# Performance work log

Measured on AMD Instinct MI355X. Metric: run time of the kernel, lower is better.

The kernel has to match this reference:

```python
import jax, jax.numpy as jnp
import numpy as np

B, C, W, H = 2, 64, 96, 96


def _conv1x1(Wm, b, x):
    # 1x1 conv == per-pixel channel mixing: (O,C) x (B,C,W,H) -> (B,O,W,H)
    return jnp.einsum('oc,bchw->bohw', Wm, x) + b[None, :, None, None]


def setup_inputs() -> dict:
    key = jax.random.key(0)
    ks = jax.random.split(key, 12)
    s = 1.0 / np.sqrt(C)
    inp = {
        'x': jax.random.normal(ks[0], (B, C, W, H), jnp.float32),
        'y': jax.random.normal(ks[1], (B, C, W, H), jnp.float32),
        'Wq': jax.random.normal(ks[2], (C, C), jnp.float32) * s,
        'bq': jax.random.normal(ks[3], (C,), jnp.float32) * 0.01,
        'Wk': jax.random.normal(ks[4], (C, C), jnp.float32) * s,
        'bk': jax.random.normal(ks[5], (C,), jnp.float32) * 0.01,
        'Wvx': jax.random.normal(ks[6], (C, C), jnp.float32) * s,
        'bvx': jax.random.normal(ks[7], (C,), jnp.float32) * 0.01,
        'Wvy': jax.random.normal(ks[8], (C, C), jnp.float32) * s,
        'bvy': jax.random.normal(ks[9], (C,), jnp.float32) * 0.01,
        'gamma': jax.random.normal(ks[10], (1,), jnp.float32) * 0.1,
        'beta': jax.random.normal(ks[11], (1,), jnp.float32) * 0.1,
    }
    return inp


def reference(x, y, Wq, bq, Wk, bk, Wvx, bvx, Wvy, bvy, gamma, beta):
    b, c, w, h = x.shape
    n = w * h
    # Q from y, K from x (cross-query structure of the original module)
    q = _conv1x1(Wq, bq, y).reshape(b, c, n)          # (B,C,N)
    k = _conv1x1(Wk, bk, x).reshape(b, c, n)          # (B,C,N)
    energy = jnp.einsum('bcm,bcn->bmn', q, k)         # (B,N,N), query rows m
    attention = jax.nn.softmax(energy, axis=-1)       # softmax over keys n
    vx = _conv1x1(Wvx, bvx, x).reshape(b, c, n)       # (B,C,N)
    vy = _conv1x1(Wvy, bvy, y).reshape(b, c, n)
    # torch: bmm(value, attention^T) -> out[:, :, m] = sum_n value[:, :, n] * att[m, n]
    out_x = jnp.einsum('bcn,bmn->bcm', vx, attention).reshape(b, c, w, h)
    out_y = jnp.einsum('bcn,bmn->bcm', vy, attention).reshape(b, c, w, h)
    x_att = gamma[0] * out_x
    y_att = beta[0] * out_y
    return (x_att, y_att)
```

## Files before the change

### kernel.cpp

```cpp
#include <hip/hip_runtime.h>
#include <cstdint>
#include <cstddef>

#define BN 2
#define CC 64
#define NN 9216
#define KT 64
#define L2E 1.44269504088896340736f
#define M0L2 63.478581798f

typedef __attribute__((ext_vector_type(8))) _Float16 half8;
typedef __attribute__((ext_vector_type(2))) __fp16 fp16x2;
typedef __attribute__((ext_vector_type(8))) short s16x8;
typedef __attribute__((ext_vector_type(4))) float f32x4;
typedef unsigned short u16;
typedef unsigned int u32;

__device__ __forceinline__ u16 f2h(float f) {
  union { _Float16 h; u16 u; } c; c.h = (_Float16)f; return c.u;
}
__device__ __forceinline__ u32 pack2h(float a, float b) {
  return (u32)f2h(a) | ((u32)f2h(b) << 16);
}
__device__ __forceinline__ u16 f2bf(float f) {
  union { float f; u32 u; } c; c.f = f;
  u32 u = c.u + 0x7FFFu + ((c.u >> 16) & 1u);
  return (u16)(u >> 16);
}
__device__ __forceinline__ half8 cvt8(f32x4 lo, f32x4 hi) {
  union { half8 v; fp16x2 p[4]; } u;
  u.p[0] = __builtin_amdgcn_cvt_pkrtz(lo[0], lo[1]);
  u.p[1] = __builtin_amdgcn_cvt_pkrtz(lo[2], lo[3]);
  u.p[2] = __builtin_amdgcn_cvt_pkrtz(hi[0], hi[1]);
  u.p[3] = __builtin_amdgcn_cvt_pkrtz(hi[2], hi[3]);
  return u.v;
}
__device__ __forceinline__ u32 cvtpk_bf16(float lo, float hi) {
  u32 r;
  asm("v_cvt_pk_bf16_f32 %0, %1, %2" : "=v"(r) : "v"(lo), "v"(hi));
  return r;
}
#if __has_builtin(__builtin_amdgcn_exp2f)
__device__ __forceinline__ float fexp2(float x) {
  return __builtin_amdgcn_exp2f(x);
}
#else
__device__ __forceinline__ float fexp2(float x) {
  float r;
  asm("v_exp_f32 %0, %1" : "=v"(r) : "v"(x));
  return r;
}
#endif
__device__ __forceinline__ void cp16(const u16* g, u16* l) {
  __builtin_amdgcn_global_load_lds(
      (const __attribute__((address_space(1))) u32*)g,
      (__attribute__((address_space(3))) u32*)l, 16, 0, 0);
}
__device__ __forceinline__ int permk(int r) {
  return (r & 0x23) | ((r & 0x0C) << 1) | ((r & 0x10) >> 2);
}

__global__ __launch_bounds__(256) void conv_mfma_kernel(
    const float* __restrict__ x, const float* __restrict__ y,
    const float* __restrict__ Wq, const float* __restrict__ bq,
    const float* __restrict__ Wk, const float* __restrict__ bk,
    const float* __restrict__ Wvx, const float* __restrict__ bvx,
    const float* __restrict__ Wvy, const float* __restrict__ bvy,
    u16* __restrict__ qkv) {
  const int cv = blockIdx.y;
  const int b = blockIdx.z;
  const int p0 = blockIdx.x * 128;
  const int tid = threadIdx.x;
  const int lane = tid & 63;
  const int wv = tid >> 6;
  const int l15 = lane & 15;
  const int h = lane >> 4;

  const float* src = (cv == 1 || cv == 2) ? x : y;
  const float* Wm = cv == 0 ? Wq : (cv == 1 ? Wk : (cv == 2 ? Wvx : Wvy));
  const float* bv = cv == 0 ? bq : (cv == 1 ? bk : (cv == 2 ? bvx : bvy));
  const float wsc = (cv == 0) ? L2E : 1.0f;
  u16* dst = qkv + (size_t)cv * ((size_t)BN * NN * CC);

  __shared__ u16 Tr[128 * 72];

  half8 wf[4][2];
#pragma unroll
  for (int ob = 0; ob < 4; ++ob)
#pragma unroll
    for (int kc = 0; kc < 2; ++kc) {
      const float* wr = Wm + (16 * ob + l15) * 64 + 32 * kc + 8 * h;
      f32x4 lo = *(const f32x4*)wr * wsc;
      f32x4 hi = *(const f32x4*)(wr + 4) * wsc;
      wf[ob][kc] = cvt8(lo, hi);
    }

  f32x4 acc[2][4];
#pragma unroll
  for (int ob = 0; ob < 4; ++ob) {
    f32x4 bias = *(const f32x4*)(bv + 16 * ob + 4 * h) * wsc;
#pragma unroll
    for (int pt = 0; pt < 2; ++pt) acc[pt][ob] = bias;
  }

  const float* xbase = src + (size_t)b * CC * NN;
#pragma unroll
  for (int pt = 0; pt < 2; ++pt) {
    const int px = p0 + 32 * wv + 16 * pt + l15;
    half8 xf[2];
#pragma unroll
    for (int kc = 0; kc < 2; ++kc) {
      const float* xp = xbase + (size_t)(32 * kc + 8 * h) * NN + px;
      float s[8];
#pragma unroll
      for (int j = 0; j < 8; ++j) s[j] = xp[(size_t)j * NN];
      xf[kc] = cvt8((f32x4){s[0], s[1], s[2], s[3]},
                    (f32x4){s[4], s[5], s[6], s[7]});
    }
#pragma unroll
    for (int ob = 0; ob < 4; ++ob) {
      acc[pt][ob] = __builtin_amdgcn_mfma_f32_16x16x32_f16(wf[ob][0], xf[0], acc[pt][ob], 0, 0, 0);
      acc[pt][ob] = __builtin_amdgcn_mfma_f32_16x16x32_f16(wf[ob][1], xf[1], acc[pt][ob], 0, 0, 0);
    }
  }

  if (cv >= 2) {
#pragma unroll
    for (int pt = 0; pt < 2; ++pt)
#pragma unroll
      for (int ob = 0; ob < 4; ++ob)
#pragma unroll
        for (int r = 0; r < 4; ++r)
          dst[((size_t)b * CC + 16 * ob + 4 * h + r) * NN +
              p0 + 32 * wv + 16 * pt + l15] = f2bf(acc[pt][ob][r]);
  } else {
#pragma unroll
    for (int pt = 0; pt < 2; ++pt) {
      const int pxl = 32 * wv + 16 * pt + l15;
#pragma unroll
      for (int ob = 0; ob < 4; ++ob) {
        uint2 v;
        v.x = pack2h(acc[pt][ob][0], acc[pt][ob][1]);
        v.y = pack2h(acc[pt][ob][2], acc[pt][ob][3]);
        *(uint2*)(Tr + pxl * 72 + 16 * ob + 4 * h) = v;
      }
    }
    __syncthreads();
    const int row = tid >> 1;
    const int hf = tid & 1;
    const uint4* s4 = (const uint4*)(Tr + row * 72) + hf * 4;
    uint4* d4 = (uint4*)(dst + ((size_t)b * NN + p0 + row) * CC) + hf * 4;
#pragma unroll
    for (int i = 0; i < 4; ++i) d4[i] = s4[i];
  }
}

#define TILE_OFF(R, c0) ((((R) * 8) + ((c0) ^ ((R) & 7))) * 8)

template <int SP>
__global__ __launch_bounds__(256, 3) void flash_kernel(
    const u16* __restrict__ qkv, float* __restrict__ accX,
    float* __restrict__ accY, float* __restrict__ ml) {
  constexpr int KPS = NN / SP;
  constexpr int STEPS = KPS / KT;
  constexpr size_t VSTRIDE = (size_t)BN * NN * CC;
  constexpr int BUF = 64 * 64;
  const int tid = threadIdx.x;
  const int lane = tid & 63;
  const int wv = tid >> 6;
  const int l15 = lane & 15;
  const int h = lane >> 4;
  const int s = blockIdx.y;
  const int b = blockIdx.z;
  const int m0w = blockIdx.x * 128 + wv * 32;

  const u16* Qt = qkv;
  const u16* Kt = qkv + (size_t)1 * BN * NN * CC;
  const u16* Vx = qkv + (size_t)2 * BN * NN * CC;

  __shared__ u16 Klds[2][BUF];
  __shared__ u16 Vxlds[2][BUF];
  __shared__ u16 Vylds[2][BUF];

  const u16* kp[2];
  const u16* vxp[2];
  int koff[2];
#pragma unroll
  for (int it = 0; it < 2; ++it) {
    const int i = tid + it * 256;
    const int r = i >> 3, cc = i & 7;
    const int sc = (cc ^ (r & 7)) * 8;
    kp[it]  = Kt + ((size_t)b * NN + s * KPS + permk(r)) * CC + sc;
    vxp[it] = Vx + ((size_t)b * CC + r) * NN + s * KPS + sc;
    koff[it] = i * 8;
  }

#pragma unroll
  for (int it = 0; it < 2; ++it) {
    cp16(kp[it], (u16*)Klds + koff[it]);
    cp16(vxp[it], (u16*)Vxlds + koff[it]);
    cp16(vxp[it] + VSTRIDE, (u16*)Vylds + koff[it]);
    kp[it] += (size_t)KT * CC;
    vxp[it] += KT;
  }

  half8 qf[2][2];
#pragma unroll
  for (int mb = 0; mb < 2; ++mb)
#pragma unroll
    for (int ch = 0; ch < 2; ++ch)
      qf[mb][ch] = *(const half8*)(Qt + ((size_t)b * NN + m0w + 16 * mb + l15) * CC +
                                   32 * ch + 8 * h);

  f32x4 oX[4][2], oY[4][2];
  float lsum[2] = {0.f, 0.f};
#pragma unroll
  for (int cb = 0; cb < 4; ++cb)
#pragma unroll
    for (int mb = 0; mb < 2; ++mb) {
      oX[cb][mb] = (f32x4){0.f, 0.f, 0.f, 0.f};
      oY[cb][mb] = (f32x4){0.f, 0.f, 0.f, 0.f};
    }

  int cur = 0;
#pragma unroll 1
  for (int step = 0; step < STEPS; ++step) {
    asm volatile("s_waitcnt vmcnt(0)" ::: "memory");
    __builtin_amdgcn_s_barrier();
    asm volatile("" ::: "memory");

    if (step + 1 < STEPS) {
      const int nsel = (cur ^ 1) * BUF;
#pragma unroll
      for (int it = 0; it < 2; ++it) {
        cp16(kp[it], (u16*)Klds + nsel + koff[it]);
        cp16(vxp[it], (u16*)Vxlds + nsel + koff[it]);
        cp16(vxp[it] + VSTRIDE, (u16*)Vylds + nsel + koff[it]);
        kp[it] += (size_t)KT * CC;
        vxp[it] += KT;
      }
    }

    const u16* kbase = (const u16*)Klds + cur * BUF;
    const u16* vxbase = (const u16*)Vxlds + cur * BUF;
    const u16* vybase = (const u16*)Vylds + cur * BUF;

    f32x4 st[2][4];
    __builtin_amdgcn_s_setprio(1);
#pragma unroll
    for (int nb = 0; nb < 4; ++nb) {
      int R = 16 * nb + l15;
      half8 kf0 = *(const half8*)(kbase + TILE_OFF(R, h));
      half8 kf1 = *(const half8*)(kbase + TILE_OFF(R, 4 + h));
#pragma unroll
      for (int mb = 0; mb < 2; ++mb) {
        f32x4 a = (f32x4){-M0L2, -M0L2, -M0L2, -M0L2};
        a = __builtin_amdgcn_mfma_f32_16x16x32_f16(kf0, qf[mb][0], a, 0, 0, 0);
        a = __builtin_amdgcn_mfma_f32_16x16x32_f16(kf1, qf[mb][1], a, 0, 0, 0);
        st[mb][nb] = a;
      }
    }
    __builtin_amdgcn_s_setprio(0);

    s16x8 pf[2][2];
#pragma unroll
    for (int mb = 0; mb < 2; ++mb) {
      union { s16x8 v; u32 w[4]; } pu[2];
      float ls = 0.f;
#pragma unroll
      for (int nb = 0; nb < 4; ++nb) {
        float p0 = fexp2(st[mb][nb][0]);
        float p1 = fexp2(st[mb][nb][1]);
        float p2 = fexp2(st[mb][nb][2]);
        float p3 = fexp2(st[mb][nb][3]);
        ls += (p0 + p1) + (p2 + p3);
        pu[nb >> 1].w[(nb & 1) * 2]     = cvtpk_bf16(p0, p1);
        pu[nb >> 1].w[(nb & 1) * 2 + 1] = cvtpk_bf16(p2, p3);
      }
      lsum[mb] += ls;
      pf[mb][0] = pu[0].v;
      pf[mb][1] = pu[1].v;
    }

    __builtin_amdgcn_s_setprio(1);
#pragma unroll
    for (int cb = 0; cb < 4; ++cb) {
      int R = 16 * cb + l15;
#pragma unroll
      for (int kc = 0; kc < 2; ++kc) {
        s16x8 bx = *(const s16x8*)(vxbase + TILE_OFF(R, 4 * kc + h));
        s16x8 by = *(const s16x8*)(vybase + TILE_OFF(R, 4 * kc + h));
#pragma unroll
        for (int mb = 0; mb < 2; ++mb) {
          oX[cb][mb] = __builtin_amdgcn_mfma_f32_16x16x32_bf16(pf[mb][kc], bx, oX[cb][mb], 0, 0, 0);
          oY[cb][mb] = __builtin_amdgcn_mfma_f32_16x16x32_bf16(pf[mb][kc], by, oY[cb][mb], 0, 0, 0);
        }
      }
    }
    __builtin_amdgcn_s_setprio(0);

    cur ^= 1;
  }

  const size_t bs = (size_t)b * SP + s;
#pragma unroll
  for (int mb = 0; mb < 2; ++mb) {
    lsum[mb] += __shfl_xor(lsum[mb], 16);
    lsum[mb] += __shfl_xor(lsum[mb], 32);
    if (h == 0) ml[bs * NN + m0w + 16 * mb + l15] = lsum[mb];
  }
#pragma unroll
  for (int mb = 0; mb < 2; ++mb) {
#pragma unroll
    for (int r = 0; r < 4; ++r) {
      const int m = m0w + 16 * mb + 4 * h + r;
#pragma unroll
      for (int cb = 0; cb < 4; ++cb) {
        accX[(bs * NN + m) * CC + 16 * cb + l15] = oX[cb][mb][r];
        accY[(bs * NN + m) * CC + 16 * cb + l15] = oY[cb][mb][r];
      }
    }
  }
}

template <int SP>
__global__ __launch_bounds__(256) void combine_kernel(
    const float* __restrict__ accX, const float* __restrict__ accY,
    const float* __restrict__ ml, const float* __restrict__ gbuf,
    const float* __restrict__ bbuf, float* __restrict__ out) {
  const int tid = threadIdx.x;
  const int b = blockIdx.x / 288;
  const int m0 = (blockIdx.x % 288) * 32;
  __shared__ float lX[64][33];
  __shared__ float lY[64][33];
  {
    const int mi = tid >> 3;
    const int c0 = (tid & 7) * 8;
    const int m = m0 + mi;
    float L = 0.f;
#pragma unroll
    for (int sp = 0; sp < SP; ++sp)
      L += ml[((size_t)b * SP + sp) * NN + m];
    const float invL = 1.0f / L;
    const float ga = gbuf[0] * invL;
    const float be = bbuf[0] * invL;
    f32x4 xv0 = (f32x4){0.f, 0.f, 0.f, 0.f}, xv1 = xv0, yv0 = xv0, yv1 = xv0;
#pragma unroll
    for (int sp = 0; sp < SP; ++sp) {
      size_t off = (((size_t)b * SP + sp) * NN + m) * CC + c0;
      xv0 += *(const f32x4*)(accX + off);
      xv1 += *(const f32x4*)(accX + off + 4);
      yv0 += *(const f32x4*)(accY + off);
      yv1 += *(const f32x4*)(accY + off + 4);
    }
#pragma unroll
    for (int r = 0; r < 4; ++r) {
      lX[c0 + r][mi] = xv0[r] * ga;
      lX[c0 + 4 + r][mi] = xv1[r] * ga;
      lY[c0 + r][mi] = yv0[r] * be;
      lY[c0 + 4 + r][mi] = yv1[r] * be;
    }
  }
  __syncthreads();
  {
    const int c = tid >> 2;
    const int mq = (tid & 3) * 8;
    float* ox = out + ((size_t)b * CC + c) * NN + m0 + mq;
    float* oy = ox + (size_t)BN * CC * NN;
    f32x4 vx0, vx1, vy0, vy1;
#pragma unroll
    for (int r = 0; r < 4; ++r) {
      vx0[r] = lX[c][mq + r];
      vx1[r] = lX[c][mq + 4 + r];
      vy0[r] = lY[c][mq + r];
      vy1[r] = lY[c][mq + 4 + r];
    }
    *(f32x4*)ox = vx0;
    *(f32x4*)(ox + 4) = vx1;
    *(f32x4*)oy = vy0;
    *(f32x4*)(oy + 4) = vy1;
  }
}

extern "C" void kernel_launch(void* const* d_in, const int* in_sizes, int n_in,
                              void* d_out, int out_size, void* d_ws, size_t ws_size,
                              hipStream_t stream) {
  const float* x   = (const float*)d_in[0];
  const float* y   = (const float*)d_in[1];
  const float* Wq  = (const float*)d_in[2];
  const float* bq  = (const float*)d_in[3];
  const float* Wk  = (const float*)d_in[4];
  const float* bk  = (const float*)d_in[5];
  const float* Wvx = (const float*)d_in[6];
  const float* bvx = (const float*)d_in[7];
  const float* Wvy = (const float*)d_in[8];
  const float* bvy = (const float*)d_in[9];
  const float* ga  = (const float*)d_in[10];
  const float* be  = (const float*)d_in[11];

  const size_t qkv_bytes = (size_t)4 * BN * NN * CC * 2;

  conv_mfma_kernel<<<dim3(72, 4, 2), 256, 0, stream>>>(x, y, Wq, bq, Wk, bk,
                                                       Wvx, bvx, Wvy, bvy,
                                                       (u16*)d_ws);

  u16* qkv = (u16*)d_ws;
  float* accX = (float*)((char*)d_ws + qkv_bytes);
  float* accY = accX + (size_t)BN * 4 * NN * CC;
  float* mlb  = accY + (size_t)BN * 4 * NN * CC;
  flash_kernel<4><<<dim3(72, 4, BN), 256, 0, stream>>>(qkv, accX, accY, mlb);
  combine_kernel<4><<<dim3(576), 256, 0, stream>>>(accX, accY, mlb, ga, be,
                                                   (float*)d_out);
}
```

Measured before the change: 181.7 us.

## Store split-K partials as bf16 and double the key split count

The flash kernel now writes its per-split output accumulators as bf16 instead of fp32. The combine kernel unpacks them back to fp32 before summing. The key-dimension split goes from 4 to 8, doubling the grid to 1152 blocks for more parallelism, and halving partial precision keeps the partial-buffer traffic roughly unchanged. The cost is bf16 rounding error in the partial sums and more per-split overhead.

```diff
diff --git a/kernel.cpp b/kernel.cpp
--- a/kernel.cpp
+++ b/kernel.cpp
@@ -26,6 +26,12 @@
   union { float f; u32 u; } c; c.f = f;
   u32 u = c.u + 0x7FFFu + ((c.u >> 16) & 1u);
   return (u16)(u >> 16);
+}
+__device__ __forceinline__ float bfl(u32 w) {
+  union { u32 u; float f; } c; c.u = w << 16; return c.f;
+}
+__device__ __forceinline__ float bfh(u32 w) {
+  union { u32 u; float f; } c; c.u = w & 0xffff0000u; return c.f;
 }
 __device__ __forceinline__ half8 cvt8(f32x4 lo, f32x4 hi) {
   union { half8 v; fp16x2 p[4]; } u;
@@ -159,8 +165,8 @@
 
 template <int SP>
 __global__ __launch_bounds__(256, 3) void flash_kernel(
-    const u16* __restrict__ qkv, float* __restrict__ accX,
-    float* __restrict__ accY, float* __restrict__ ml) {
+    const u16* __restrict__ qkv, u16* __restrict__ accX,
+    u16* __restrict__ accY, float* __restrict__ ml) {
   constexpr int KPS = NN / SP;
   constexpr int STEPS = KPS / KT;
   constexpr size_t VSTRIDE = (size_t)BN * NN * CC;
@@ -316,8 +322,8 @@
       const int m = m0w + 16 * mb + 4 * h + r;
 #pragma unroll
       for (int cb = 0; cb < 4; ++cb) {
-        accX[(bs * NN + m) * CC + 16 * cb + l15] = oX[cb][mb][r];
-        accY[(bs * NN + m) * CC + 16 * cb + l15] = oY[cb][mb][r];
+        accX[(bs * NN + m) * CC + 16 * cb + l15] = f2bf(oX[cb][mb][r]);
+        accY[(bs * NN + m) * CC + 16 * cb + l15] = f2bf(oY[cb][mb][r]);
       }
     }
   }
@@ -325,7 +331,7 @@
 
 template <int SP>
 __global__ __launch_bounds__(256) void combine_kernel(
-    const float* __restrict__ accX, const float* __restrict__ accY,
+    const u16* __restrict__ accX, const u16* __restrict__ accY,
     const float* __restrict__ ml, const float* __restrict__ gbuf,
     const float* __restrict__ bbuf, float* __restrict__ out) {
   const int tid = threadIdx.x;
@@ -348,10 +354,16 @@
 #pragma unroll
     for (int sp = 0; sp < SP; ++sp) {
       size_t off = (((size_t)b * SP + sp) * NN + m) * CC + c0;
-      xv0 += *(const f32x4*)(accX + off);
-      xv1 += *(const f32x4*)(accX + off + 4);
-      yv0 += *(const f32x4*)(accY + off);
-      yv1 += *(const f32x4*)(accY + off + 4);
+      uint4 hx = *(const uint4*)(accX + off);
+      uint4 hy = *(const uint4*)(accY + off);
+      xv0[0] += bfl(hx.x); xv0[1] += bfh(hx.x);
+      xv0[2] += bfl(hx.y); xv0[3] += bfh(hx.y);
+      xv1[0] += bfl(hx.z); xv1[1] += bfh(hx.z);
+      xv1[2] += bfl(hx.w); xv1[3] += bfh(hx.w);
+      yv0[0] += bfl(hy.x); yv0[1] += bfh(hy.x);
+      yv0[2] += bfl(hy.y); yv0[3] += bfh(hy.y);
+      yv1[0] += bfl(hy.z); yv1[1] += bfh(hy.z);
+      yv1[2] += bfl(hy.w); yv1[3] += bfh(hy.w);
     }
 #pragma unroll
     for (int r = 0; r < 4; ++r) {
@@ -405,10 +417,10 @@
                                                        (u16*)d_ws);
 
   u16* qkv = (u16*)d_ws;
-  float* accX = (float*)((char*)d_ws + qkv_bytes);
-  float* accY = accX + (size_t)BN * 4 * NN * CC;
-  float* mlb  = accY + (size_t)BN * 4 * NN * CC;
-  flash_kernel<4><<<dim3(72, 4, BN), 256, 0, stream>>>(qkv, accX, accY, mlb);
-  combine_kernel<4><<<dim3(576), 256, 0, stream>>>(accX, accY, mlb, ga, be,
+  u16* accX = (u16*)((char*)d_ws + qkv_bytes);
+  u16* accY = accX + (size_t)BN * 8 * NN * CC;
+  float* mlb = (float*)(accY + (size_t)BN * 8 * NN * CC);
+  flash_kernel<8><<<dim3(72, 8, BN), 256, 0, stream>>>(qkv, accX, accY, mlb);
+  combine_kernel<8><<<dim3(576), 256, 0, stream>>>(accX, accY, mlb, ga, be,
                                                    (float*)d_out);
 }
```

New measurement: 168.1 us. -7.5%, faster.
